# Kernel tuning notes

Measured on AMD Instinct MI355X. Metric: run time of the kernel, lower is better.

## Reference

```python
import jax, jax.numpy as jnp
import numpy as np

VOXEL = 0.8  # meters per grid cell (from `* 0.8` and `/0.8` in source)
GRID = 256   # BEV grid size (from torch.zeros(256, 256))


def _points_in_any_box(points, boxes):
    """points: (M, 3) grid-cell coords shared across batch; boxes: (B, T, 7) as
    (cx, cy, cz, dx, dy, dz, yaw). Returns (B, M) bool: point inside any box.
    Mirrors roiaware_pool3d points_in_boxes_gpu (rotate by -yaw, half-size test)."""
    shift = points[None, :, None, :] - boxes[:, None, :, :3]      # (B, M, T, 3)
    c = jnp.cos(boxes[:, None, :, 6])                              # (B, 1, T)
    s = jnp.sin(boxes[:, None, :, 6])
    rx = shift[..., 0] * c + shift[..., 1] * s                     # local x
    ry = -shift[..., 0] * s + shift[..., 1] * c                    # local y
    half = boxes[:, None, :, 3:6] * 0.5                            # (B, 1, T, 3)
    inb = (jnp.abs(rx) < half[..., 0]) \
        & (jnp.abs(ry) < half[..., 1]) \
        & (jnp.abs(shift[..., 2]) <= half[..., 2])                 # (B, M, T)
    return jnp.any(inb, axis=-1)                                   # (B, M)


def setup_inputs() -> dict:
    key = jax.random.key(0)
    k1, k2, k3, k4, k5, k6 = jax.random.split(key, 6)
    B, C, H, T = 16, 32, GRID, 20
    u1 = jax.random.uniform(k1, (B, C, H, H))
    added = jnp.where(u1 > 0.98, u1, 0.0)
    u2 = jax.random.uniform(k2, (B, C + 1, H, H))
    orig = jnp.where(u2 > 0.98, u2, 0.0)
    # boxes inside the grid extent [0, 256*0.8) meters
    ctr = jax.random.uniform(k3, (B, T, 2), minval=40.0, maxval=160.0)
    cz = jnp.full((B, T, 1), VOXEL)
    dims = jax.random.uniform(k4, (B, T, 3), minval=4.0, maxval=16.0)
    dims = dims.at[..., 2].set(2.0)  # dz covers the fixed point z = 0.8
    yaw = jax.random.uniform(k5, (B, T, 1), minval=-3.14, maxval=3.14)
    boxes = jnp.concatenate([ctr, cz, dims, yaw], axis=-1)
    tf_ego = jax.random.normal(k6, (B, 4, 4))
    return {"added_points": added, "original_points": orig,
            "boxes": boxes, "tf_ego": tf_ego}


def reference(added_points, original_points, boxes, tf_ego):
    B, _, H, W = added_points.shape
    T = boxes.shape[1]
    # collapse channel/height dim -> BEV occupancy maps (B, H, W)
    pred = jnp.sum(added_points, axis=1)
    orig = jnp.sum(original_points[:, 1:], axis=1)
    # every grid cell is a candidate point at (i*0.8, j*0.8, 0.8) (source: nonzero idx * 0.8)
    ii, jj = jnp.meshgrid(jnp.arange(H), jnp.arange(W), indexing='ij')
    pts = jnp.stack([ii.reshape(-1) * VOXEL,
                     jj.reshape(-1) * VOXEL,
                     jnp.full((H * W,), VOXEL)], axis=-1).astype(boxes.dtype)
    in_box = _points_in_any_box(pts, boxes)                        # (B, H*W)
    # keep only occupied cells that fall inside some box -> binary grids
    occ_p = (pred.reshape(B, -1) != 0) & in_box
    occ_o = (orig.reshape(B, -1) != 0) & in_box
    inter = jnp.sum(occ_p & occ_o, axis=-1).astype(jnp.float32)
    union = jnp.sum(occ_p | occ_o, axis=-1).astype(jnp.float32)
    iou_b = inter / jnp.maximum(union, 1.0)                        # per-batch grid IoU
    # source accumulates the (identical) IoU once per box, then divides by batch
    return T * jnp.sum(iou_b) / B
```

## Files before the change

kernel.cpp:

```cpp
#include <hip/hip_runtime.h>
#include <hip/hip_bf16.h>
#include <cstdint>

#define H 256
#define HW (H * H)
#define T_BOX 20
#define CPT 8
#define BLOCK 256
#define CELLS_PER_BLOCK (BLOCK * CPT)
#define BLOCKS_PER_BATCH (HW / CELLS_PER_BLOCK)

__device__ __forceinline__ float bf2f(unsigned short u) {
    union { unsigned int x; float f; } c;
    c.x = ((unsigned int)u) << 16;
    return c.f;
}
__device__ __forceinline__ unsigned short f2bf_bits(float x) {
    union { float f; unsigned int u; } c;
    c.f = x;
    return (unsigned short)((c.u + 0x7fffu + ((c.u >> 16) & 1u)) >> 16);
}
__device__ __forceinline__ float bfq(float x) { return bf2f(f2bf_bits(x)); }

__global__ __launch_bounds__(BLOCK)
void occ_iou_kernel(const void* __restrict__ added_,
                    const void* __restrict__ orig_,
                    const void* __restrict__ boxes_,
                    unsigned long long* __restrict__ ws,
                    int Ca, int Co) {
    __shared__ float s_cx[T_BOX], s_cy[T_BOX], s_sn[T_BOX], s_cs[T_BOX],
                     s_hx[T_BOX], s_hy[T_BOX];

    const int b     = blockIdx.x >> 5;
    const int chunk = blockIdx.x & 31;
    const int t     = threadIdx.x;

    const float* bxf = (const float*)boxes_;
    const bool is_f32 = (fabsf(bxf[2] - 0.8f) < 0.25f) &&
                        (fabsf(bxf[9] - 0.8f) < 0.25f);

    if (t < T_BOX) {
        float cx, cy, cz, dx, dy, dz, yaw, pz;
        if (is_f32) {
            const float* bp = bxf + ((size_t)b * T_BOX + t) * 7;
            cx = bp[0]; cy = bp[1]; cz = bp[2];
            dx = bp[3]; dy = bp[4]; dz = bp[5]; yaw = bp[6];
            pz = 0.8f;
        } else {
            const unsigned short* bp =
                (const unsigned short*)boxes_ + ((size_t)b * T_BOX + t) * 7;
            cx = bf2f(bp[0]); cy = bf2f(bp[1]); cz = bf2f(bp[2]);
            dx = bf2f(bp[3]); dy = bf2f(bp[4]); dz = bf2f(bp[5]);
            yaw = bf2f(bp[6]);
            pz = bfq(0.8f);
        }
        float hx = 0.5f * dx, hy = 0.5f * dy, hz = 0.5f * dz;
        if (!(fabsf(pz - cz) <= hz)) hx = -1.0f;
        s_cx[t] = cx; s_cy[t] = cy;
        s_sn[t] = sinf(yaw); s_cs[t] = cosf(yaw);
        s_hx[t] = hx; s_hy[t] = hy;
    }
    __syncthreads();

    const int m0 = chunk * CELLS_PER_BLOCK + t * CPT;
    const int i  = m0 >> 8;
    const int j0 = m0 & 255;

    float px = (float)((double)i * 0.8);
    float py[CPT];
#pragma unroll
    for (int e = 0; e < CPT; ++e) py[e] = (float)((double)(j0 + e) * 0.8);
    if (!is_f32) {
        px = bfq(px);
#pragma unroll
        for (int e = 0; e < CPT; ++e) py[e] = bfq(py[e]);
    }

    unsigned int pm = 0, om = 0;
    if (is_f32) {
        const uint4* pa = (const uint4*)((const float*)added_ +
                                         (size_t)b * Ca * HW + m0);
        uint4 a0 = make_uint4(0,0,0,0), a1 = make_uint4(0,0,0,0);
#pragma unroll 8
        for (int c = 0; c < Ca; ++c) {
            uint4 v0 = pa[(size_t)c * (HW / 4)];
            uint4 v1 = pa[(size_t)c * (HW / 4) + 1];
            a0.x |= v0.x; a0.y |= v0.y; a0.z |= v0.z; a0.w |= v0.w;
            a1.x |= v1.x; a1.y |= v1.y; a1.z |= v1.z; a1.w |= v1.w;
        }
        const uint4* po = (const uint4*)((const float*)orig_ +
                                         ((size_t)b * Co + 1) * HW + m0);
        uint4 b0 = make_uint4(0,0,0,0), b1 = make_uint4(0,0,0,0);
#pragma unroll 8
        for (int c = 0; c < Co - 1; ++c) {
            uint4 v0 = po[(size_t)c * (HW / 4)];
            uint4 v1 = po[(size_t)c * (HW / 4) + 1];
            b0.x |= v0.x; b0.y |= v0.y; b0.z |= v0.z; b0.w |= v0.w;
            b1.x |= v1.x; b1.y |= v1.y; b1.z |= v1.z; b1.w |= v1.w;
        }
        unsigned int pw[8] = {a0.x,a0.y,a0.z,a0.w,a1.x,a1.y,a1.z,a1.w};
        unsigned int ow[8] = {b0.x,b0.y,b0.z,b0.w,b1.x,b1.y,b1.z,b1.w};
#pragma unroll
        for (int e = 0; e < CPT; ++e) {
            pm |= (pw[e] != 0u) << e;
            om |= (ow[e] != 0u) << e;
        }
    } else {
        const uint4* pa = (const uint4*)((const unsigned short*)added_ +
                                         (size_t)b * Ca * HW + m0);
        uint4 accp = make_uint4(0,0,0,0);
#pragma unroll 8
        for (int c = 0; c < Ca; ++c) {
            uint4 v = pa[(size_t)c * (HW / 8)];
            accp.x |= v.x; accp.y |= v.y; accp.z |= v.z; accp.w |= v.w;
        }
        const uint4* po = (const uint4*)((const unsigned short*)orig_ +
                                         ((size_t)b * Co + 1) * HW + m0);
        uint4 acco = make_uint4(0,0,0,0);
#pragma unroll 8
        for (int c = 0; c < Co - 1; ++c) {
            uint4 v = po[(size_t)c * (HW / 8)];
            acco.x |= v.x; acco.y |= v.y; acco.z |= v.z; acco.w |= v.w;
        }
        union { uint4 v; unsigned short u[8]; } Up, Uo;
        Up.v = accp; Uo.v = acco;
#pragma unroll
        for (int e = 0; e < CPT; ++e) {
            pm |= (Up.u[e] != 0) << e;
            om |= (Uo.u[e] != 0) << e;
        }
    }

    unsigned int inb = 0;
#pragma unroll 4
    for (int k = 0; k < T_BOX; ++k) {
        const float cx = s_cx[k], cy = s_cy[k], sn = s_sn[k], cs = s_cs[k];
        const float hx = s_hx[k], hy = s_hy[k];
        const float sx  = px - cx;
        const float sxc = sx * cs, sxs = sx * sn;
#pragma unroll
        for (int e = 0; e < CPT; ++e) {
            const float sy = py[e] - cy;
            const float rx = sxc + sy * sn;
            const float ry = sy * cs - sxs;
            if ((fabsf(rx) < hx) & (fabsf(ry) < hy)) inb |= (1u << e);
        }
    }

    const unsigned int inter = __popc(pm & om & inb);
    const unsigned int uni   = __popc((pm | om) & inb);

    unsigned long long val = ((unsigned long long)inter << 32) |
                             (unsigned long long)uni;
#pragma unroll
    for (int off = 32; off > 0; off >>= 1)
        val += __shfl_down(val, off, 64);

    if ((t & 63) == 0) atomicAdd(&ws[b], val);
}

__global__ void finish_kernel(const unsigned long long* __restrict__ ws,
                              unsigned int* __restrict__ out, int B, int T) {
    if (threadIdx.x == 0 && blockIdx.x == 0) {
        float s = 0.0f;
        for (int b = 0; b < B; ++b) {
            unsigned long long v = ws[b];
            float inter = (float)(unsigned int)(v >> 32);
            float uni   = (float)(unsigned int)(v & 0xffffffffu);
            s += inter / fmaxf(uni, 1.0f);
        }
        const float x = (float)T * s / (float)B;
        const unsigned int h = f2bf_bits(x);
        out[0] = (h << 16) | h;
    }
}

extern "C" void kernel_launch(void* const* d_in, const int* in_sizes, int n_in,
                              void* d_out, int out_size, void* d_ws, size_t ws_size,
                              hipStream_t stream) {
    const void* added = d_in[0];
    const void* orig  = d_in[1];
    const void* boxes = d_in[2];

    const int B  = in_sizes[2] / (T_BOX * 7);
    const int Ca = in_sizes[0] / (B * HW);
    const int Co = in_sizes[1] / (B * HW);

    unsigned long long* ws = (unsigned long long*)d_ws;
    hipMemsetAsync(ws, 0, (size_t)B * sizeof(unsigned long long), stream);

    occ_iou_kernel<<<B * BLOCKS_PER_BATCH, BLOCK, 0, stream>>>(
        added, orig, boxes, ws, Ca, Co);
    finish_kernel<<<1, 64, 0, stream>>>(ws, (unsigned int*)d_out, B, T_BOX);
}
```

Baseline: 293.7 us.

## Split channel reduction across four wavefronts per block and combine via shared memory

```diff
diff --git a/kernel.cpp b/kernel.cpp
--- a/kernel.cpp
+++ b/kernel.cpp
@@ -5,10 +5,10 @@
 #define H 256
 #define HW (H * H)
 #define T_BOX 20
-#define CPT 8
 #define BLOCK 256
-#define CELLS_PER_BLOCK (BLOCK * CPT)
-#define BLOCKS_PER_BATCH (HW / CELLS_PER_BLOCK)
+#define CHUNK_CELLS 512
+#define CHUNKS (HW / CHUNK_CELLS)
+#define CGRP 4
 
 __device__ __forceinline__ float bf2f(unsigned short u) {
     union { unsigned int x; float f; } c;
@@ -30,10 +30,13 @@
                     int Ca, int Co) {
     __shared__ float s_cx[T_BOX], s_cy[T_BOX], s_sn[T_BOX], s_cs[T_BOX],
                      s_hx[T_BOX], s_hy[T_BOX];
-
-    const int b     = blockIdx.x >> 5;
-    const int chunk = blockIdx.x & 31;
+    __shared__ unsigned int s_pm[CGRP][64], s_om[CGRP][64];
+
+    const int b     = blockIdx.x >> 7;
+    const int chunk = blockIdx.x & (CHUNKS - 1);
     const int t     = threadIdx.x;
+    const int g     = t >> 6;
+    const int s     = t & 63;
 
     const float* bxf = (const float*)boxes_;
     const bool is_f32 = (fabsf(bxf[2] - 0.8f) < 0.25f) &&
@@ -60,29 +63,16 @@
         s_sn[t] = sinf(yaw); s_cs[t] = cosf(yaw);
         s_hx[t] = hx; s_hy[t] = hy;
     }
-    __syncthreads();
-
-    const int m0 = chunk * CELLS_PER_BLOCK + t * CPT;
-    const int i  = m0 >> 8;
-    const int j0 = m0 & 255;
-
-    float px = (float)((double)i * 0.8);
-    float py[CPT];
-#pragma unroll
-    for (int e = 0; e < CPT; ++e) py[e] = (float)((double)(j0 + e) * 0.8);
-    if (!is_f32) {
-        px = bfq(px);
-#pragma unroll
-        for (int e = 0; e < CPT; ++e) py[e] = bfq(py[e]);
-    }
-
-    unsigned int pm = 0, om = 0;
+
+    const int m0 = chunk * CHUNK_CELLS + s * 8;
+    unsigned int pm8 = 0, om8 = 0;
+
     if (is_f32) {
         const uint4* pa = (const uint4*)((const float*)added_ +
                                          (size_t)b * Ca * HW + m0);
         uint4 a0 = make_uint4(0,0,0,0), a1 = make_uint4(0,0,0,0);
 #pragma unroll 8
-        for (int c = 0; c < Ca; ++c) {
+        for (int c = g; c < Ca; c += CGRP) {
             uint4 v0 = pa[(size_t)c * (HW / 4)];
             uint4 v1 = pa[(size_t)c * (HW / 4) + 1];
             a0.x |= v0.x; a0.y |= v0.y; a0.z |= v0.z; a0.w |= v0.w;
@@ -92,7 +82,7 @@
                                          ((size_t)b * Co + 1) * HW + m0);
         uint4 b0 = make_uint4(0,0,0,0), b1 = make_uint4(0,0,0,0);
 #pragma unroll 8
-        for (int c = 0; c < Co - 1; ++c) {
+        for (int c = g; c < Co - 1; c += CGRP) {
             uint4 v0 = po[(size_t)c * (HW / 4)];
             uint4 v1 = po[(size_t)c * (HW / 4) + 1];
             b0.x |= v0.x; b0.y |= v0.y; b0.z |= v0.z; b0.w |= v0.w;
@@ -101,62 +91,82 @@
         unsigned int pw[8] = {a0.x,a0.y,a0.z,a0.w,a1.x,a1.y,a1.z,a1.w};
         unsigned int ow[8] = {b0.x,b0.y,b0.z,b0.w,b1.x,b1.y,b1.z,b1.w};
 #pragma unroll
-        for (int e = 0; e < CPT; ++e) {
-            pm |= (pw[e] != 0u) << e;
-            om |= (ow[e] != 0u) << e;
+        for (int e = 0; e < 8; ++e) {
+            pm8 |= (unsigned int)(pw[e] != 0u) << e;
+            om8 |= (unsigned int)(ow[e] != 0u) << e;
         }
     } else {
-        const uint4* pa = (const uint4*)((const unsigned short*)added_ +
-                                         (size_t)b * Ca * HW + m0);
+        const unsigned short* pa0 = (const unsigned short*)added_ +
+                                    (size_t)b * Ca * HW + m0;
         uint4 accp = make_uint4(0,0,0,0);
 #pragma unroll 8
-        for (int c = 0; c < Ca; ++c) {
-            uint4 v = pa[(size_t)c * (HW / 8)];
+        for (int c = g; c < Ca; c += CGRP) {
+            uint4 v = *(const uint4*)(pa0 + (size_t)c * HW);
             accp.x |= v.x; accp.y |= v.y; accp.z |= v.z; accp.w |= v.w;
         }
-        const uint4* po = (const uint4*)((const unsigned short*)orig_ +
-                                         ((size_t)b * Co + 1) * HW + m0);
+        const unsigned short* po0 = (const unsigned short*)orig_ +
+                                    ((size_t)b * Co + 1) * HW + m0;
         uint4 acco = make_uint4(0,0,0,0);
 #pragma unroll 8
-        for (int c = 0; c < Co - 1; ++c) {
-            uint4 v = po[(size_t)c * (HW / 8)];
+        for (int c = g; c < Co - 1; c += CGRP) {
+            uint4 v = *(const uint4*)(po0 + (size_t)c * HW);
             acco.x |= v.x; acco.y |= v.y; acco.z |= v.z; acco.w |= v.w;
         }
         union { uint4 v; unsigned short u[8]; } Up, Uo;
         Up.v = accp; Uo.v = acco;
 #pragma unroll
-        for (int e = 0; e < CPT; ++e) {
-            pm |= (Up.u[e] != 0) << e;
-            om |= (Uo.u[e] != 0) << e;
-        }
-    }
-
-    unsigned int inb = 0;
+        for (int e = 0; e < 8; ++e) {
+            pm8 |= (unsigned int)(Up.u[e] != 0) << e;
+            om8 |= (unsigned int)(Uo.u[e] != 0) << e;
+        }
+    }
+    s_pm[g][s] = pm8; s_om[g][s] = om8;
+    __syncthreads();
+
+    if (t < 64) {
+        const unsigned int pm = s_pm[0][t] | s_pm[1][t] | s_pm[2][t] | s_pm[3][t];
+        const unsigned int om = s_om[0][t] | s_om[1][t] | s_om[2][t] | s_om[3][t];
+
+        const int M  = chunk * CHUNK_CELLS + t * 8;
+        const int i  = M >> 8;
+        const int j0 = M & 255;
+        float px = (float)((double)i * 0.8);
+        float py[8];
+#pragma unroll
+        for (int e = 0; e < 8; ++e) py[e] = (float)((double)(j0 + e) * 0.8);
+        if (!is_f32) {
+            px = bfq(px);
+#pragma unroll
+            for (int e = 0; e < 8; ++e) py[e] = bfq(py[e]);
+        }
+
+        unsigned int inb = 0;
 #pragma unroll 4
-    for (int k = 0; k < T_BOX; ++k) {
-        const float cx = s_cx[k], cy = s_cy[k], sn = s_sn[k], cs = s_cs[k];
-        const float hx = s_hx[k], hy = s_hy[k];
-        const float sx  = px - cx;
-        const float sxc = sx * cs, sxs = sx * sn;
-#pragma unroll
-        for (int e = 0; e < CPT; ++e) {
-            const float sy = py[e] - cy;
-            const float rx = sxc + sy * sn;
-            const float ry = sy * cs - sxs;
-            if ((fabsf(rx) < hx) & (fabsf(ry) < hy)) inb |= (1u << e);
-        }
-    }
-
-    const unsigned int inter = __popc(pm & om & inb);
-    const unsigned int uni   = __popc((pm | om) & inb);
-
-    unsigned long long val = ((unsigned long long)inter << 32) |
-                             (unsigned long long)uni;
-#pragma unroll
-    for (int off = 32; off > 0; off >>= 1)
-        val += __shfl_down(val, off, 64);
-
-    if ((t & 63) == 0) atomicAdd(&ws[b], val);
+        for (int k = 0; k < T_BOX; ++k) {
+            const float cx = s_cx[k], cy = s_cy[k], sn = s_sn[k], cs = s_cs[k];
+            const float hx = s_hx[k], hy = s_hy[k];
+            const float sx  = px - cx;
+            const float sxc = sx * cs, sxs = sx * sn;
+#pragma unroll
+            for (int e = 0; e < 8; ++e) {
+                const float sy = py[e] - cy;
+                const float rx = sxc + sy * sn;
+                const float ry = sy * cs - sxs;
+                if ((fabsf(rx) < hx) & (fabsf(ry) < hy)) inb |= (1u << e);
+            }
+        }
+
+        const unsigned int inter = __popc(pm & om & inb);
+        const unsigned int uni   = __popc((pm | om) & inb);
+
+        unsigned long long val = ((unsigned long long)inter << 32) |
+                                 (unsigned long long)uni;
+#pragma unroll
+        for (int off = 32; off > 0; off >>= 1)
+            val += __shfl_down(val, off, 64);
+
+        if (t == 0) atomicAdd(&ws[b], val);
+    }
 }
 
 __global__ void finish_kernel(const unsigned long long* __restrict__ ws,
@@ -189,7 +199,7 @@
     unsigned long long* ws = (unsigned long long*)d_ws;
     hipMemsetAsync(ws, 0, (size_t)B * sizeof(unsigned long long), stream);
 
-    occ_iou_kernel<<<B * BLOCKS_PER_BATCH, BLOCK, 0, stream>>>(
+    occ_iou_kernel<<<B * CHUNKS, BLOCK, 0, stream>>>(
         added, orig, boxes, ws, Ca, Co);
     finish_kernel<<<1, 64, 0, stream>>>(ws, (unsigned int*)d_out, B, T_BOX);
 }
```

Measured after the change: 289.1 us. Within noise of the previous version (-1.6%).

## Split occupancy reduction into per-channel bitmap pass with atomicOr, then IoU pass

Applied to the files above, without the earlier changes.

```diff
diff --git a/kernel.cpp b/kernel.cpp
--- a/kernel.cpp
+++ b/kernel.cpp
@@ -5,10 +5,11 @@
 #define H 256
 #define HW (H * H)
 #define T_BOX 20
-#define CPT 8
-#define BLOCK 256
-#define CELLS_PER_BLOCK (BLOCK * CPT)
-#define BLOCKS_PER_BATCH (HW / CELLS_PER_BLOCK)
+#define SLICES 8
+#define SPAN 32
+#define BCELLS 4096
+#define BBLK (HW / BCELLS)
+#define WPB 2048
 
 __device__ __forceinline__ float bf2f(unsigned short u) {
     union { unsigned int x; float f; } c;
@@ -22,27 +23,87 @@
 }
 __device__ __forceinline__ float bfq(float x) { return bf2f(f2bf_bits(x)); }
 
-__global__ __launch_bounds__(BLOCK)
-void occ_iou_kernel(const void* __restrict__ added_,
-                    const void* __restrict__ orig_,
-                    const void* __restrict__ boxes_,
-                    unsigned long long* __restrict__ ws,
-                    int Ca, int Co) {
+__device__ __forceinline__ bool detect_f32(const void* boxes_) {
+    const float* bxf = (const float*)boxes_;
+    return (fabsf(bxf[2] - 0.8f) < 0.25f) && (fabsf(bxf[9] - 0.8f) < 0.25f);
+}
+
+__global__ __launch_bounds__(256)
+void occ_bitmap_kernel(const void* __restrict__ added_,
+                       const void* __restrict__ orig_,
+                       const void* __restrict__ boxes_,
+                       unsigned int* __restrict__ mapP,
+                       unsigned int* __restrict__ mapO,
+                       int B, int Ca, int Co) {
+    const bool is_f32 = detect_f32(boxes_);
+
+    const int m     = blockIdx.x >> 3;
+    const int s8    = blockIdx.x & (SLICES - 1);
+    const int t     = threadIdx.x;
+    const int cell0 = s8 * (HW / SLICES) + t * SPAN;
+
+    size_t src_cell;
+    unsigned int* dst;
+    int b;
+    if (m < B * Ca) {
+        b = m / Ca;
+        src_cell = (size_t)m * HW;
+        dst = mapP;
+    } else {
+        const int m2 = m - B * Ca;
+        b = m2 / (Co - 1);
+        const int c2 = m2 - b * (Co - 1);
+        src_cell = ((size_t)b * Co + 1 + c2) * HW;
+        dst = mapO;
+    }
+    const void* src = (m < B * Ca) ? added_ : orig_;
+
+    unsigned int mask = 0;
+    if (is_f32) {
+        const uint4* p = (const uint4*)((const float*)src + src_cell + cell0);
+        uint4 w[8];
+#pragma unroll
+        for (int q = 0; q < 8; ++q) w[q] = p[q];
+#pragma unroll
+        for (int q = 0; q < 8; ++q) {
+            mask |= (unsigned int)(w[q].x != 0u) << (4 * q + 0);
+            mask |= (unsigned int)(w[q].y != 0u) << (4 * q + 1);
+            mask |= (unsigned int)(w[q].z != 0u) << (4 * q + 2);
+            mask |= (unsigned int)(w[q].w != 0u) << (4 * q + 3);
+        }
+    } else {
+        const uint4* p = (const uint4*)((const unsigned short*)src + src_cell + cell0);
+        uint4 w[4];
+#pragma unroll
+        for (int q = 0; q < 4; ++q) w[q] = p[q];
+        union { uint4 v[4]; unsigned short u[32]; } U;
+#pragma unroll
+        for (int q = 0; q < 4; ++q) U.v[q] = w[q];
+#pragma unroll
+        for (int e = 0; e < 32; ++e)
+            mask |= (unsigned int)(U.u[e] != 0) << e;
+    }
+
+    if (mask) atomicOr(&dst[(size_t)b * WPB + (cell0 >> 5)], mask);
+}
+
+__global__ __launch_bounds__(256)
+void iou_kernel(const unsigned int* __restrict__ mapP,
+                const unsigned int* __restrict__ mapO,
+                const void* __restrict__ boxes_,
+                unsigned long long* __restrict__ cnt) {
     __shared__ float s_cx[T_BOX], s_cy[T_BOX], s_sn[T_BOX], s_cs[T_BOX],
                      s_hx[T_BOX], s_hy[T_BOX];
 
-    const int b     = blockIdx.x >> 5;
-    const int chunk = blockIdx.x & 31;
-    const int t     = threadIdx.x;
-
-    const float* bxf = (const float*)boxes_;
-    const bool is_f32 = (fabsf(bxf[2] - 0.8f) < 0.25f) &&
-                        (fabsf(bxf[9] - 0.8f) < 0.25f);
+    const int cb = blockIdx.x & (BBLK - 1);
+    const int b  = blockIdx.x >> 4;
+    const int t  = threadIdx.x;
+    const bool is_f32 = detect_f32(boxes_);
 
     if (t < T_BOX) {
         float cx, cy, cz, dx, dy, dz, yaw, pz;
         if (is_f32) {
-            const float* bp = bxf + ((size_t)b * T_BOX + t) * 7;
+            const float* bp = (const float*)boxes_ + ((size_t)b * T_BOX + t) * 7;
             cx = bp[0]; cy = bp[1]; cz = bp[2];
             dx = bp[3]; dy = bp[4]; dz = bp[5]; yaw = bp[6];
             pz = 0.8f;
@@ -62,84 +123,32 @@
     }
     __syncthreads();
 
-    const int m0 = chunk * CELLS_PER_BLOCK + t * CPT;
-    const int i  = m0 >> 8;
-    const int j0 = m0 & 255;
-
+    const int M = cb * BCELLS + t * 16;
+    const unsigned int w  = ((unsigned int)b << 11) + ((unsigned int)M >> 5);
+    const unsigned int sh = (unsigned int)M & 31u;
+    const unsigned int pm = (mapP[w] >> sh) & 0xFFFFu;
+    const unsigned int om = (mapO[w] >> sh) & 0xFFFFu;
+
+    const int i  = M >> 8;
+    const int j0 = M & 255;
     float px = (float)((double)i * 0.8);
-    float py[CPT];
-#pragma unroll
-    for (int e = 0; e < CPT; ++e) py[e] = (float)((double)(j0 + e) * 0.8);
+    float py[16];
+#pragma unroll
+    for (int e = 0; e < 16; ++e) py[e] = (float)((double)(j0 + e) * 0.8);
     if (!is_f32) {
         px = bfq(px);
 #pragma unroll
-        for (int e = 0; e < CPT; ++e) py[e] = bfq(py[e]);
-    }
-
-    unsigned int pm = 0, om = 0;
-    if (is_f32) {
-        const uint4* pa = (const uint4*)((const float*)added_ +
-                                         (size_t)b * Ca * HW + m0);
-        uint4 a0 = make_uint4(0,0,0,0), a1 = make_uint4(0,0,0,0);
-#pragma unroll 8
-        for (int c = 0; c < Ca; ++c) {
-            uint4 v0 = pa[(size_t)c * (HW / 4)];
-            uint4 v1 = pa[(size_t)c * (HW / 4) + 1];
-            a0.x |= v0.x; a0.y |= v0.y; a0.z |= v0.z; a0.w |= v0.w;
-            a1.x |= v1.x; a1.y |= v1.y; a1.z |= v1.z; a1.w |= v1.w;
-        }
-        const uint4* po = (const uint4*)((const float*)orig_ +
-                                         ((size_t)b * Co + 1) * HW + m0);
-        uint4 b0 = make_uint4(0,0,0,0), b1 = make_uint4(0,0,0,0);
-#pragma unroll 8
-        for (int c = 0; c < Co - 1; ++c) {
-            uint4 v0 = po[(size_t)c * (HW / 4)];
-            uint4 v1 = po[(size_t)c * (HW / 4) + 1];
-            b0.x |= v0.x; b0.y |= v0.y; b0.z |= v0.z; b0.w |= v0.w;
-            b1.x |= v1.x; b1.y |= v1.y; b1.z |= v1.z; b1.w |= v1.w;
-        }
-        unsigned int pw[8] = {a0.x,a0.y,a0.z,a0.w,a1.x,a1.y,a1.z,a1.w};
-        unsigned int ow[8] = {b0.x,b0.y,b0.z,b0.w,b1.x,b1.y,b1.z,b1.w};
-#pragma unroll
-        for (int e = 0; e < CPT; ++e) {
-            pm |= (pw[e] != 0u) << e;
-            om |= (ow[e] != 0u) << e;
-        }
-    } else {
-        const uint4* pa = (const uint4*)((const unsigned short*)added_ +
-                                         (size_t)b * Ca * HW + m0);
-        uint4 accp = make_uint4(0,0,0,0);
-#pragma unroll 8
-        for (int c = 0; c < Ca; ++c) {
-            uint4 v = pa[(size_t)c * (HW / 8)];
-            accp.x |= v.x; accp.y |= v.y; accp.z |= v.z; accp.w |= v.w;
-        }
-        const uint4* po = (const uint4*)((const unsigned short*)orig_ +
-                                         ((size_t)b * Co + 1) * HW + m0);
-        uint4 acco = make_uint4(0,0,0,0);
-#pragma unroll 8
-        for (int c = 0; c < Co - 1; ++c) {
-            uint4 v = po[(size_t)c * (HW / 8)];
-            acco.x |= v.x; acco.y |= v.y; acco.z |= v.z; acco.w |= v.w;
-        }
-        union { uint4 v; unsigned short u[8]; } Up, Uo;
-        Up.v = accp; Uo.v = acco;
-#pragma unroll
-        for (int e = 0; e < CPT; ++e) {
-            pm |= (Up.u[e] != 0) << e;
-            om |= (Uo.u[e] != 0) << e;
-        }
+        for (int e = 0; e < 16; ++e) py[e] = bfq(py[e]);
     }
 
     unsigned int inb = 0;
-#pragma unroll 4
     for (int k = 0; k < T_BOX; ++k) {
         const float cx = s_cx[k], cy = s_cy[k], sn = s_sn[k], cs = s_cs[k];
         const float hx = s_hx[k], hy = s_hy[k];
         const float sx  = px - cx;
         const float sxc = sx * cs, sxs = sx * sn;
 #pragma unroll
-        for (int e = 0; e < CPT; ++e) {
+        for (int e = 0; e < 16; ++e) {
             const float sy = py[e] - cy;
             const float rx = sxc + sy * sn;
             const float ry = sy * cs - sxs;
@@ -156,15 +165,15 @@
     for (int off = 32; off > 0; off >>= 1)
         val += __shfl_down(val, off, 64);
 
-    if ((t & 63) == 0) atomicAdd(&ws[b], val);
-}
-
-__global__ void finish_kernel(const unsigned long long* __restrict__ ws,
+    if ((t & 63) == 0) atomicAdd(&cnt[b], val);
+}
+
+__global__ void finish_kernel(const unsigned long long* __restrict__ cnt,
                               unsigned int* __restrict__ out, int B, int T) {
     if (threadIdx.x == 0 && blockIdx.x == 0) {
         float s = 0.0f;
         for (int b = 0; b < B; ++b) {
-            unsigned long long v = ws[b];
+            unsigned long long v = cnt[b];
             float inter = (float)(unsigned int)(v >> 32);
             float uni   = (float)(unsigned int)(v & 0xffffffffu);
             s += inter / fmaxf(uni, 1.0f);
@@ -186,10 +195,14 @@
     const int Ca = in_sizes[0] / (B * HW);
     const int Co = in_sizes[1] / (B * HW);
 
-    unsigned long long* ws = (unsigned long long*)d_ws;
-    hipMemsetAsync(ws, 0, (size_t)B * sizeof(unsigned long long), stream);
-
-    occ_iou_kernel<<<B * BLOCKS_PER_BATCH, BLOCK, 0, stream>>>(
-        added, orig, boxes, ws, Ca, Co);
-    finish_kernel<<<1, 64, 0, stream>>>(ws, (unsigned int*)d_out, B, T_BOX);
-}
+    unsigned int* mapP = (unsigned int*)d_ws;
+    unsigned int* mapO = mapP + (size_t)B * WPB;
+    unsigned long long* cnt = (unsigned long long*)(mapO + (size_t)B * WPB);
+    hipMemsetAsync(d_ws, 0, (size_t)B * WPB * 8 + (size_t)B * 8, stream);
+
+    const int n_maps = B * Ca + B * (Co - 1);
+    occ_bitmap_kernel<<<n_maps * SLICES, 256, 0, stream>>>(
+        added, orig, boxes, mapP, mapO, B, Ca, Co);
+    iou_kernel<<<B * BBLK, 256, 0, stream>>>(mapP, mapO, boxes, cnt);
+    finish_kernel<<<1, 64, 0, stream>>>(cnt, (unsigned int*)d_out, B, T_BOX);
+}
```

New measurement: 296.1 us. Within noise of the previous version (+0.8%).
